# Kernel optimization log

Measured on AMD Instinct MI355X. Metric: run time of the kernel, lower is better.

Reference implementation:

```python
import jax, jax.numpy as jnp
import numpy as np

D_MODEL = 1024
NUM_HEADS = 16
D_K = D_MODEL // NUM_HEADS
SCALE = float(np.sqrt(D_K))


def setup_inputs() -> dict:
    key = jax.random.key(0)
    ks = jax.random.split(key, 9)
    B, S = 4, 2048
    x = jax.random.normal(ks[0], (B, S, D_MODEL), dtype=jnp.float32)
    init = 1.0 / np.sqrt(D_MODEL)
    def lin(kw, kb):
        W = jax.random.uniform(kw, (D_MODEL, D_MODEL), jnp.float32, -init, init)
        b = jax.random.uniform(kb, (D_MODEL,), jnp.float32, -init, init)
        return W, b
    Wq, bq = lin(ks[1], ks[2])
    Wk, bk = lin(ks[3], ks[4])
    Wv, bv = lin(ks[5], ks[6])
    Wo, bo = lin(ks[7], ks[8])
    return {"x": x, "Wq": Wq, "bq": bq, "Wk": Wk, "bk": bk,
            "Wv": Wv, "bv": bv, "Wo": Wo, "bo": bo}


def reference(x, Wq, bq, Wk, bk, Wv, bv, Wo, bo):
    B, S, _ = x.shape
    # projections (torch Linear: y = x @ W.T + b)
    q = x @ Wq.T + bq
    k = x @ Wk.T + bk
    v = x @ Wv.T + bv
    # [B, H, S, d_k]
    q = q.reshape(B, S, NUM_HEADS, D_K).transpose(0, 2, 1, 3)
    k = k.reshape(B, S, NUM_HEADS, D_K).transpose(0, 2, 1, 3)
    v = v.reshape(B, S, NUM_HEADS, D_K).transpose(0, 2, 1, 3)
    # explicit scores [B, H, S, S]
    scores = jnp.einsum('bhqd,bhkd->bhqk', q, k) / SCALE
    attn = jax.nn.softmax(scores, axis=-1)
    # dropout is identity in eval mode
    ctx = jnp.einsum('bhqk,bhkd->bhqd', attn, v)
    ctx = ctx.transpose(0, 2, 1, 3).reshape(B, S, D_MODEL)
    return ctx @ Wo.T + bo
```

## Files before the change

### kernel.cpp

```cpp
#include <hip/hip_runtime.h>
#include <stdint.h>


typedef __attribute__((ext_vector_type(8))) short short8;
typedef __attribute__((ext_vector_type(4))) float f32x4;
typedef __attribute__((ext_vector_type(16))) float f32x16;
typedef __attribute__((ext_vector_type(4))) unsigned int u32x4;
typedef unsigned short ushort_t;
typedef unsigned int uint_t;

#define DMODEL 1024
#define SEQ 2048
#define NH 16
#define QSCALE 0.18033688011112043f

__device__ __forceinline__ ushort_t bfbits(float f) {
  uint32_t u = __float_as_uint(f);
  u = (u + 0x7fffu + ((u >> 16) & 1u)) >> 16;
  return (ushort_t)u;
}
__device__ __forceinline__ uint_t cvt_pk_bf16(float lo, float hi) {
  uint_t r;
  asm("v_cvt_pk_bf16_f32 %0, %1, %2" : "=v"(r) : "v"(lo), "v"(hi));
  return r;
}
__device__ __forceinline__ float exp2_hw(float x) {
  float r;
  asm("v_exp_f32 %0, %1" : "=v"(r) : "v"(x));
  return r;
}
__device__ __forceinline__ f32x16 mfma32(short8 a, short8 b, f32x16 c) {
  return __builtin_amdgcn_mfma_f32_32x32x16_bf16(a, b, c, 0, 0, 0);
}

typedef __attribute__((address_space(1))) void gvoid_t;
typedef __attribute__((address_space(3))) void lvoid_t;
__device__ __forceinline__ void gl_lds16(const void* gp, void* lp) {
  __builtin_amdgcn_global_load_lds((gvoid_t*)(uintptr_t)gp, (lvoid_t*)lp, 16, 0, 0);
}

__global__ __launch_bounds__(256) void cvt_bf16(const float* __restrict__ in,
                                                ushort_t* __restrict__ out) {
  int i = (int)(blockIdx.x * 256u + threadIdx.x) * 8;
  const float4* p = (const float4*)(in + i);
  float4 a = p[0], b = p[1];
  short8 o;
  o[0] = (short)bfbits(a.x); o[1] = (short)bfbits(a.y);
  o[2] = (short)bfbits(a.z); o[3] = (short)bfbits(a.w);
  o[4] = (short)bfbits(b.x); o[5] = (short)bfbits(b.y);
  o[6] = (short)bfbits(b.z); o[7] = (short)bfbits(b.w);
  *(short8*)(out + i) = o;
}

__global__ __launch_bounds__(256) void cvt4_bf16(const float* __restrict__ w0,
                                                 const float* __restrict__ w1,
                                                 const float* __restrict__ w2,
                                                 const float* __restrict__ w3,
                                                 ushort_t* __restrict__ out) {
  int which = (int)(blockIdx.x >> 9);
  const float* src = (which == 0) ? w0 : (which == 1) ? w1 : (which == 2) ? w2 : w3;
  int i = (int)(((blockIdx.x & 511) * 256u) + threadIdx.x) * 8;
  const float4* p = (const float4*)(src + i);
  float4 a = p[0], b = p[1];
  short8 o;
  o[0] = (short)bfbits(a.x); o[1] = (short)bfbits(a.y);
  o[2] = (short)bfbits(a.z); o[3] = (short)bfbits(a.w);
  o[4] = (short)bfbits(b.x); o[5] = (short)bfbits(b.y);
  o[6] = (short)bfbits(b.z); o[7] = (short)bfbits(b.w);
  *(short8*)(out + (size_t)which * 1048576 + i) = o;
}

#define EPI_QKV 0
#define EPI_OUT 1

template <int EPI>
__global__ __launch_bounds__(256) void gemm_bt(const ushort_t* __restrict__ A,
                                               const ushort_t* __restrict__ Bw,
                                               const float* __restrict__ b0,
                                               const float* __restrict__ b1,
                                               const float* __restrict__ b2,
                                               ushort_t* __restrict__ Qb,
                                               ushort_t* __restrict__ Kb,
                                               ushort_t* __restrict__ Vtb,
                                               float* __restrict__ Yf) {
  __shared__ alignas(16) ushort_t As[2][128 * 32];
  __shared__ alignas(16) ushort_t Bs[2][128 * 32];
  const int tid = threadIdx.x;
  const int lane = tid & 63, w = tid >> 6;
  const int g = lane >> 4, r16 = lane & 15;
  const int wr = w >> 1, wc = w & 1;

  int nwg = (int)(gridDim.x * gridDim.y);
  int flat = (int)(blockIdx.x + gridDim.x * blockIdx.y);
  int cpx = nwg >> 3;
  int sw = (flat & 7) * cpx + (flat >> 3);
  const int bm0 = (sw & 63) * 128;
  const int bn0 = (sw >> 6) * 128;

  f32x4 acc[4][4];
#pragma unroll
  for (int m = 0; m < 4; ++m)
#pragma unroll
    for (int n = 0; n < 4; ++n) acc[m][n] = (f32x4){0.f, 0.f, 0.f, 0.f};

  const int srow = tid >> 2;
  const int sc = (tid & 3) * 8;

  auto stage = [&](int bf, int k0) {
    char* AsB = (char*)As[bf];
    char* BsB = (char*)Bs[bf];
    gl_lds16(A + (size_t)(bm0 + srow) * DMODEL + k0 + sc, AsB + w * 1024);
    gl_lds16(A + (size_t)(bm0 + 64 + srow) * DMODEL + k0 + sc, AsB + w * 1024 + 4096);
    gl_lds16(Bw + (size_t)(bn0 + srow) * DMODEL + k0 + sc, BsB + w * 1024);
    gl_lds16(Bw + (size_t)(bn0 + 64 + srow) * DMODEL + k0 + sc, BsB + w * 1024 + 4096);
  };

  stage(0, 0);
  int cur = 0;
  for (int k0 = 0; k0 < DMODEL; k0 += 32) {
    if (k0 < DMODEL - 32) {
      stage(cur ^ 1, k0 + 32);
      asm volatile("s_waitcnt vmcnt(4)\n\ts_barrier" ::: "memory");
    } else {
      asm volatile("s_waitcnt vmcnt(0)\n\ts_barrier" ::: "memory");
    }
    const char* AsB = (const char*)As[cur];
    const char* BsB = (const char*)Bs[cur];

    short8 af[4], bfr[4];
#pragma unroll
    for (int m = 0; m < 4; ++m)
      af[m] = *(const short8*)(AsB + (wr * 64 + m * 16 + r16) * 64 + g * 16);
#pragma unroll
    for (int n = 0; n < 4; ++n)
      bfr[n] = *(const short8*)(BsB + (wc * 64 + n * 16 + r16) * 64 + g * 16);
    __builtin_amdgcn_s_setprio(1);
#pragma unroll
    for (int m = 0; m < 4; ++m)
#pragma unroll
      for (int n = 0; n < 4; ++n)
        acc[m][n] = __builtin_amdgcn_mfma_f32_16x16x32_bf16(af[m], bfr[n], acc[m][n], 0, 0, 0);
    __builtin_amdgcn_s_setprio(0);
    asm volatile("s_waitcnt lgkmcnt(0)\n\ts_barrier" ::: "memory");
    cur ^= 1;
  }

  if (EPI == EPI_OUT) {
    float bv[4];
#pragma unroll
    for (int n = 0; n < 4; ++n) bv[n] = b0[bn0 + wc * 64 + n * 16 + r16];
#pragma unroll
    for (int m = 0; m < 4; ++m)
#pragma unroll
      for (int r = 0; r < 4; ++r) {
        int grow = bm0 + wr * 64 + m * 16 + 4 * g + r;
        float* orow = Yf + (size_t)grow * DMODEL + bn0 + wc * 64;
#pragma unroll
        for (int n = 0; n < 4; ++n) orow[n * 16 + r16] = acc[m][n][r] + bv[n];
      }
  } else {
    int mat = bn0 >> 10;
    const float* bias = (mat == 0) ? b0 : (mat == 1 ? b1 : b2);
    ushort_t* dQK = (mat == 0) ? Qb : Kb;
    int nc0 = bn0 & 1023;
    float scl = (mat == 0) ? QSCALE : 1.0f;
    float bv[4];
#pragma unroll
    for (int n = 0; n < 4; ++n) bv[n] = bias[nc0 + wc * 64 + n * 16 + r16];
#pragma unroll
    for (int m = 0; m < 4; ++m)
#pragma unroll
      for (int r = 0; r < 4; ++r) {
        int grow = bm0 + wr * 64 + m * 16 + 4 * g + r;
        int b = grow >> 11, s = grow & 2047;
#pragma unroll
        for (int n = 0; n < 4; ++n) {
          int gcl = nc0 + wc * 64 + n * 16 + r16;
          int h = gcl >> 6, d = gcl & 63;
          float vv = (acc[m][n][r] + bv[n]) * scl;
          if (mat < 2)
            dQK[((size_t)(b * NH + h) * SEQ + s) * 64 + d] = bfbits(vv);
          else
            Vtb[((size_t)(b * NH + h) * 64 + d) * SEQ + s] = bfbits(vv);
        }
      }
  }
}

__global__ __launch_bounds__(256) void attn_fwd(const ushort_t* __restrict__ Q,
                                                const ushort_t* __restrict__ K,
                                                const ushort_t* __restrict__ Vt,
                                                ushort_t* __restrict__ ctx) {
  __shared__ alignas(16) ushort_t Ks[2][64 * 64];
  __shared__ alignas(16) ushort_t Vs[2][64 * 64];
  const int tid = threadIdx.x;
  const int lane = tid & 63, w = tid >> 6;
  const int q32 = lane & 31, h = lane >> 5;

  int flat = (int)(blockIdx.x + 16 * blockIdx.y);
  int sw = (flat & 7) * 128 + (flat >> 3);
  int bh = sw >> 4, q0 = (sw & 15) * 128;

  const ushort_t* Qp = Q + (size_t)bh * SEQ * 64;
  const ushort_t* Kp = K + (size_t)bh * SEQ * 64;
  const ushort_t* Vp = Vt + (size_t)bh * 64 * SEQ;

  short8 qf[4];
  {
    const ushort_t* qr = Qp + (size_t)(q0 + w * 32 + q32) * 64 + h * 8;
    qf[0] = *(const short8*)(qr);
    qf[1] = *(const short8*)(qr + 16);
    qf[2] = *(const short8*)(qr + 32);
    qf[3] = *(const short8*)(qr + 48);
  }

  f32x16 o0 = (f32x16)0.0f, o1 = (f32x16)0.0f;
  float l = 0.f;

  const int swz = (q32 & 7) << 4;
  const char* krow0;

  auto stage = [&](int bf, int kv0) {
#pragma unroll
    for (int it = 0; it < 2; ++it) {
      int row = (tid >> 3) + it * 32;
      int cs = (tid & 7) ^ (row & 7);
      gl_lds16(Kp + (size_t)(kv0 + row) * 64 + cs * 8, (char*)Ks[bf] + w * 1024 + it * 4096);
      gl_lds16(Vp + (size_t)row * SEQ + kv0 + cs * 8, (char*)Vs[bf] + w * 1024 + it * 4096);
    }
  };

  stage(0, 0);
  int cur = 0;
  for (int t = 0; t < 32; ++t) {
    if (t < 31) {
      stage(cur ^ 1, (t + 1) * 64);
      asm volatile("s_waitcnt vmcnt(4)\n\ts_barrier" ::: "memory");
    } else {
      asm volatile("s_waitcnt vmcnt(0)\n\ts_barrier" ::: "memory");
    }
    const char* kb0 = (const char*)Ks[cur] + q32 * 128;
    const char* kb1 = kb0 + 32 * 128;
    const char* vb0 = (const char*)Vs[cur] + q32 * 128;
    const char* vb1 = vb0 + 32 * 128;

    f32x16 s0 = (f32x16)0.0f, s1 = (f32x16)0.0f;
    __builtin_amdgcn_s_setprio(1);
#pragma unroll
    for (int c = 0; c < 4; ++c) {
      short8 kf0 = *(const short8*)(kb0 + ((32 * c + 16 * h) ^ swz));
      short8 kf1 = *(const short8*)(kb1 + ((32 * c + 16 * h) ^ swz));
      s0 = mfma32(kf0, qf[c], s0);
      s1 = mfma32(kf1, qf[c], s1);
    }
    __builtin_amdgcn_s_setprio(0);

#pragma unroll
    for (int j = 0; j < 16; ++j) {
      s0[j] = exp2_hw(s0[j]);
      s1[j] = exp2_hw(s1[j]);
    }

    uint_t pw[16];
#pragma unroll
    for (int i = 0; i < 8; ++i) {
      pw[i] = cvt_pk_bf16(s0[2 * i], s0[2 * i + 1]);
      pw[8 + i] = cvt_pk_bf16(s1[2 * i], s1[2 * i + 1]);
    }
#pragma unroll
    for (int c = 0; c < 4; ++c) {
      asm volatile("v_permlane32_swap_b32 %0, %1" : "+v"(pw[4 * c]), "+v"(pw[4 * c + 2]));
      asm volatile("v_permlane32_swap_b32 %0, %1" : "+v"(pw[4 * c + 1]), "+v"(pw[4 * c + 3]));
    }

    __builtin_amdgcn_s_setprio(1);
#pragma unroll
    for (int c = 0; c < 4; ++c) {
      u32x4 pk = {pw[4 * c], pw[4 * c + 1], pw[4 * c + 2], pw[4 * c + 3]};
      short8 pfc = __builtin_bit_cast(short8, pk);
      short8 vf0 = *(const short8*)(vb0 + ((32 * c + 16 * h) ^ swz));
      short8 vf1 = *(const short8*)(vb1 + ((32 * c + 16 * h) ^ swz));
      o0 = mfma32(vf0, pfc, o0);
      o1 = mfma32(vf1, pfc, o1);
    }
    __builtin_amdgcn_s_setprio(0);

    {
      f32x16 ts = s0 + s1;
      float a = (ts[0] + ts[1]) + (ts[2] + ts[3]);
      float b = (ts[4] + ts[5]) + (ts[6] + ts[7]);
      float c2 = (ts[8] + ts[9]) + (ts[10] + ts[11]);
      float d = (ts[12] + ts[13]) + (ts[14] + ts[15]);
      l += (a + b) + (c2 + d);
    }

    asm volatile("s_waitcnt lgkmcnt(0)\n\ts_barrier" ::: "memory");
    cur ^= 1;
  }

  float ltot = l + __shfl_xor(l, 32);
  float inv = 1.0f / ltot;
  int b = bh >> 4, hd = bh & 15;
  uint_t* crow = (uint_t*)(ctx + ((size_t)(b * SEQ + q0 + w * 32 + q32)) * DMODEL + hd * 64);
#pragma unroll
  for (int i = 0; i < 8; ++i) {
    int ui = (i & 1) + 4 * (i >> 1) + 2 * h;
    crow[ui] = cvt_pk_bf16(o0[2 * i] * inv, o0[2 * i + 1] * inv);
    crow[16 + ui] = cvt_pk_bf16(o1[2 * i] * inv, o1[2 * i + 1] * inv);
  }
  (void)krow0;
}

extern "C" void kernel_launch(void* const* d_in, const int* in_sizes, int n_in,
                              void* d_out, int out_size, void* d_ws, size_t ws_size,
                              hipStream_t stream) {
  (void)in_sizes; (void)n_in; (void)out_size; (void)ws_size;
  const float* x  = (const float*)d_in[0];
  const float* Wq = (const float*)d_in[1];
  const float* bq = (const float*)d_in[2];
  const float* Wk = (const float*)d_in[3];
  const float* bk = (const float*)d_in[4];
  const float* Wv = (const float*)d_in[5];
  const float* bv = (const float*)d_in[6];
  const float* Wo = (const float*)d_in[7];
  const float* bo = (const float*)d_in[8];
  float* out = (float*)d_out;

  ushort_t* xb  = (ushort_t*)d_ws;
  ushort_t* w3  = xb + 8388608;
  ushort_t* wob = w3 + 3145728;
  ushort_t* Qb  = wob + 1048576;
  ushort_t* Kb  = Qb + 8388608;
  ushort_t* Vtb = Kb + 8388608;
  ushort_t* cx  = Vtb + 8388608;

  cvt_bf16<<<4096, 256, 0, stream>>>(x, xb);
  cvt4_bf16<<<2048, 256, 0, stream>>>(Wq, Wk, Wv, Wo, w3);

  gemm_bt<EPI_QKV><<<dim3(64, 24), 256, 0, stream>>>(xb, w3, bq, bk, bv, Qb, Kb, Vtb, nullptr);
  attn_fwd<<<dim3(16, 64), 256, 0, stream>>>(Qb, Kb, Vtb, cx);
  gemm_bt<EPI_OUT><<<dim3(64, 8), 256, 0, stream>>>(cx, wob, bo, nullptr, nullptr,
                                                    nullptr, nullptr, nullptr, out);
}
```

Measured before the change: 333.2 us.

## Triple-buffer GEMM and attention loads, widen attention blocks, MFMA row-sum

Both the projection GEMM and the attention kernel move from double to triple buffering in LDS. Each iteration now waits once, prefetches two tiles ahead, and drops the trailing barrier. The attention kernel runs 512-thread blocks covering 256 queries, so each K/V tile staged in LDS is shared by more waves. It computes the softmax denominator with an extra MFMA against a ones vector instead of scalar adds. The V-transpose epilogue packs four bf16 values into one vector store. Dropping the second barrier relies on three buffers keeping an iteration's reads clear of the buffer being overwritten.

```diff
diff --git a/kernel.cpp b/kernel.cpp
--- a/kernel.cpp
+++ b/kernel.cpp
@@ -6,6 +6,7 @@
 typedef __attribute__((ext_vector_type(4))) float f32x4;
 typedef __attribute__((ext_vector_type(16))) float f32x16;
 typedef __attribute__((ext_vector_type(4))) unsigned int u32x4;
+typedef __attribute__((ext_vector_type(4))) unsigned short us4;
 typedef unsigned short ushort_t;
 typedef unsigned int uint_t;
 
@@ -83,8 +84,8 @@
                                                ushort_t* __restrict__ Kb,
                                                ushort_t* __restrict__ Vtb,
                                                float* __restrict__ Yf) {
-  __shared__ alignas(16) ushort_t As[2][128 * 32];
-  __shared__ alignas(16) ushort_t Bs[2][128 * 32];
+  __shared__ alignas(16) ushort_t As[3][128 * 32];
+  __shared__ alignas(16) ushort_t Bs[3][128 * 32];
   const int tid = threadIdx.x;
   const int lane = tid & 63, w = tid >> 6;
   const int g = lane >> 4, r16 = lane & 15;
@@ -116,17 +117,17 @@
   };
 
   stage(0, 0);
-  int cur = 0;
-  for (int k0 = 0; k0 < DMODEL; k0 += 32) {
-    if (k0 < DMODEL - 32) {
-      stage(cur ^ 1, k0 + 32);
+  stage(1, 32);
+  int buf = 0;
+  for (int t = 0; t < 32; ++t) {
+    if (t < 31)
       asm volatile("s_waitcnt vmcnt(4)\n\ts_barrier" ::: "memory");
-    } else {
+    else
       asm volatile("s_waitcnt vmcnt(0)\n\ts_barrier" ::: "memory");
-    }
-    const char* AsB = (const char*)As[cur];
-    const char* BsB = (const char*)Bs[cur];
-
+    if (t < 30) stage((t + 2) % 3, (t + 2) * 32);
+
+    const char* AsB = (const char*)As[buf];
+    const char* BsB = (const char*)Bs[buf];
     short8 af[4], bfr[4];
 #pragma unroll
     for (int m = 0; m < 4; ++m)
@@ -141,8 +142,7 @@
       for (int n = 0; n < 4; ++n)
         acc[m][n] = __builtin_amdgcn_mfma_f32_16x16x32_bf16(af[m], bfr[n], acc[m][n], 0, 0, 0);
     __builtin_amdgcn_s_setprio(0);
-    asm volatile("s_waitcnt lgkmcnt(0)\n\ts_barrier" ::: "memory");
-    cur ^= 1;
+    buf = (buf == 2) ? 0 : buf + 1;
   }
 
   if (EPI == EPI_OUT) {
@@ -167,39 +167,54 @@
     float bv[4];
 #pragma unroll
     for (int n = 0; n < 4; ++n) bv[n] = bias[nc0 + wc * 64 + n * 16 + r16];
-#pragma unroll
-    for (int m = 0; m < 4; ++m)
-#pragma unroll
-      for (int r = 0; r < 4; ++r) {
-        int grow = bm0 + wr * 64 + m * 16 + 4 * g + r;
-        int b = grow >> 11, s = grow & 2047;
+    if (mat < 2) {
+#pragma unroll
+      for (int m = 0; m < 4; ++m)
+#pragma unroll
+        for (int r = 0; r < 4; ++r) {
+          int grow = bm0 + wr * 64 + m * 16 + 4 * g + r;
+          int b = grow >> 11, s = grow & 2047;
+#pragma unroll
+          for (int n = 0; n < 4; ++n) {
+            int gcl = nc0 + wc * 64 + n * 16 + r16;
+            int h = gcl >> 6, d = gcl & 63;
+            dQK[((size_t)(b * NH + h) * SEQ + s) * 64 + d] = bfbits((acc[m][n][r] + bv[n]) * scl);
+          }
+        }
+    } else {
+#pragma unroll
+      for (int m = 0; m < 4; ++m) {
+        int grow0 = bm0 + wr * 64 + m * 16 + 4 * g;
+        int b = grow0 >> 11, s0 = grow0 & 2047;
 #pragma unroll
         for (int n = 0; n < 4; ++n) {
           int gcl = nc0 + wc * 64 + n * 16 + r16;
           int h = gcl >> 6, d = gcl & 63;
-          float vv = (acc[m][n][r] + bv[n]) * scl;
-          if (mat < 2)
-            dQK[((size_t)(b * NH + h) * SEQ + s) * 64 + d] = bfbits(vv);
-          else
-            Vtb[((size_t)(b * NH + h) * 64 + d) * SEQ + s] = bfbits(vv);
+          us4 pk;
+          pk[0] = bfbits(acc[m][n][0] + bv[n]);
+          pk[1] = bfbits(acc[m][n][1] + bv[n]);
+          pk[2] = bfbits(acc[m][n][2] + bv[n]);
+          pk[3] = bfbits(acc[m][n][3] + bv[n]);
+          *(us4*)(Vtb + ((size_t)(b * NH + h) * 64 + d) * SEQ + s0) = pk;
         }
       }
-  }
-}
-
-__global__ __launch_bounds__(256) void attn_fwd(const ushort_t* __restrict__ Q,
-                                                const ushort_t* __restrict__ K,
-                                                const ushort_t* __restrict__ Vt,
-                                                ushort_t* __restrict__ ctx) {
-  __shared__ alignas(16) ushort_t Ks[2][64 * 64];
-  __shared__ alignas(16) ushort_t Vs[2][64 * 64];
+    }
+  }
+}
+
+__global__ __launch_bounds__(512, 4) void attn_fwd(const ushort_t* __restrict__ Q,
+                                                   const ushort_t* __restrict__ K,
+                                                   const ushort_t* __restrict__ Vt,
+                                                   ushort_t* __restrict__ ctx) {
+  __shared__ alignas(16) ushort_t Ks[3][64 * 64];
+  __shared__ alignas(16) ushort_t Vs[3][64 * 64];
   const int tid = threadIdx.x;
   const int lane = tid & 63, w = tid >> 6;
   const int q32 = lane & 31, h = lane >> 5;
 
-  int flat = (int)(blockIdx.x + 16 * blockIdx.y);
-  int sw = (flat & 7) * 128 + (flat >> 3);
-  int bh = sw >> 4, q0 = (sw & 15) * 128;
+  int flat = (int)(blockIdx.x + 8 * blockIdx.y);
+  int sw = (flat & 7) * 64 + (flat >> 3);
+  int bh = sw >> 3, q0 = (sw & 7) * 256;
 
   const ushort_t* Qp = Q + (size_t)bh * SEQ * 64;
   const ushort_t* Kp = K + (size_t)bh * SEQ * 64;
@@ -214,34 +229,33 @@
     qf[3] = *(const short8*)(qr + 48);
   }
 
-  f32x16 o0 = (f32x16)0.0f, o1 = (f32x16)0.0f;
-  float l = 0.f;
+  f32x16 o0 = (f32x16)0.0f, o1 = (f32x16)0.0f, lacc = (f32x16)0.0f;
+  short8 ones;
+#pragma unroll
+  for (int j = 0; j < 8; ++j) ones[j] = (short)0x3F80;
 
   const int swz = (q32 & 7) << 4;
-  const char* krow0;
 
   auto stage = [&](int bf, int kv0) {
-#pragma unroll
-    for (int it = 0; it < 2; ++it) {
-      int row = (tid >> 3) + it * 32;
-      int cs = (tid & 7) ^ (row & 7);
-      gl_lds16(Kp + (size_t)(kv0 + row) * 64 + cs * 8, (char*)Ks[bf] + w * 1024 + it * 4096);
-      gl_lds16(Vp + (size_t)row * SEQ + kv0 + cs * 8, (char*)Vs[bf] + w * 1024 + it * 4096);
-    }
+    int row = tid >> 3;
+    int cs = (tid & 7) ^ (row & 7);
+    gl_lds16(Kp + (size_t)(kv0 + row) * 64 + cs * 8, (char*)Ks[bf] + w * 1024);
+    gl_lds16(Vp + (size_t)row * SEQ + kv0 + cs * 8, (char*)Vs[bf] + w * 1024);
   };
 
   stage(0, 0);
-  int cur = 0;
+  stage(1, 64);
+  int buf = 0;
   for (int t = 0; t < 32; ++t) {
-    if (t < 31) {
-      stage(cur ^ 1, (t + 1) * 64);
-      asm volatile("s_waitcnt vmcnt(4)\n\ts_barrier" ::: "memory");
-    } else {
+    if (t < 31)
+      asm volatile("s_waitcnt vmcnt(2)\n\ts_barrier" ::: "memory");
+    else
       asm volatile("s_waitcnt vmcnt(0)\n\ts_barrier" ::: "memory");
-    }
-    const char* kb0 = (const char*)Ks[cur] + q32 * 128;
+    if (t < 30) stage((t + 2) % 3, (t + 2) * 64);
+
+    const char* kb0 = (const char*)Ks[buf] + q32 * 128;
     const char* kb1 = kb0 + 32 * 128;
-    const char* vb0 = (const char*)Vs[cur] + q32 * 128;
+    const char* vb0 = (const char*)Vs[buf] + q32 * 128;
     const char* vb1 = vb0 + 32 * 128;
 
     f32x16 s0 = (f32x16)0.0f, s1 = (f32x16)0.0f;
@@ -282,24 +296,14 @@
       short8 vf1 = *(const short8*)(vb1 + ((32 * c + 16 * h) ^ swz));
       o0 = mfma32(vf0, pfc, o0);
       o1 = mfma32(vf1, pfc, o1);
+      lacc = mfma32(ones, pfc, lacc);
     }
     __builtin_amdgcn_s_setprio(0);
 
-    {
-      f32x16 ts = s0 + s1;
-      float a = (ts[0] + ts[1]) + (ts[2] + ts[3]);
-      float b = (ts[4] + ts[5]) + (ts[6] + ts[7]);
-      float c2 = (ts[8] + ts[9]) + (ts[10] + ts[11]);
-      float d = (ts[12] + ts[13]) + (ts[14] + ts[15]);
-      l += (a + b) + (c2 + d);
-    }
-
-    asm volatile("s_waitcnt lgkmcnt(0)\n\ts_barrier" ::: "memory");
-    cur ^= 1;
-  }
-
-  float ltot = l + __shfl_xor(l, 32);
-  float inv = 1.0f / ltot;
+    buf = (buf == 2) ? 0 : buf + 1;
+  }
+
+  float inv = 1.0f / lacc[0];
   int b = bh >> 4, hd = bh & 15;
   uint_t* crow = (uint_t*)(ctx + ((size_t)(b * SEQ + q0 + w * 32 + q32)) * DMODEL + hd * 64);
 #pragma unroll
@@ -308,7 +312,6 @@
     crow[ui] = cvt_pk_bf16(o0[2 * i] * inv, o0[2 * i + 1] * inv);
     crow[16 + ui] = cvt_pk_bf16(o1[2 * i] * inv, o1[2 * i + 1] * inv);
   }
-  (void)krow0;
 }
 
 extern "C" void kernel_launch(void* const* d_in, const int* in_sizes, int n_in,
@@ -338,7 +341,7 @@
   cvt4_bf16<<<2048, 256, 0, stream>>>(Wq, Wk, Wv, Wo, w3);
 
   gemm_bt<EPI_QKV><<<dim3(64, 24), 256, 0, stream>>>(xb, w3, bq, bk, bv, Qb, Kb, Vtb, nullptr);
-  attn_fwd<<<dim3(16, 64), 256, 0, stream>>>(Qb, Kb, Vtb, cx);
+  attn_fwd<<<dim3(8, 64), 512, 0, stream>>>(Qb, Kb, Vtb, cx);
   gemm_bt<EPI_OUT><<<dim3(64, 8), 256, 0, stream>>>(cx, wob, bo, nullptr, nullptr,
                                                     nullptr, nullptr, nullptr, out);
 }
```

New measurement: 284.6 us. 1.17x faster.
